# Kernel tuning notes

Hardware: AMD Instinct MI355X
Metric: run time of the kernel (lower is better)

The kernel has to match this reference:

```python
import jax, jax.numpy as jnp
import numpy as np

B, T, C, H = 1, 4096, 768, 12
D = C // H  # 64


def setup_inputs() -> dict:
    key = jax.random.key(0)
    k1, k2, k3, k4, k5 = jax.random.split(key, 5)
    x = jax.random.normal(k1, (B, T, C), dtype=jnp.float32)
    # causal mask: 1.0 where attention is DISALLOWED (strict upper triangle)
    mask = (1.0 - jnp.tril(jnp.ones((T, T), dtype=jnp.float32)))[None, None, :, :]
    s_attn = 1.0 / np.sqrt(C)
    W_qkv = jax.random.normal(k2, (C, 3 * C), dtype=jnp.float32) * s_attn
    b_qkv = jnp.zeros((3 * C,), dtype=jnp.float32)
    W_proj = jax.random.normal(k3, (C, C), dtype=jnp.float32) * s_attn
    b_proj = jnp.zeros((C,), dtype=jnp.float32)
    return {"x": x, "mask": mask, "W_qkv": W_qkv, "b_qkv": b_qkv,
            "W_proj": W_proj, "b_proj": b_proj}


def reference(x, mask, W_qkv, b_qkv, W_proj, b_proj):
    qkv = jnp.einsum('btc,cf->btf', x, W_qkv) + b_qkv        # [B,T,3C]
    q, k, v = jnp.split(qkv, 3, axis=2)
    # [B,T,C] -> [B,H,T,D]
    q = q.reshape(B, T, H, D).transpose(0, 2, 1, 3)
    k = k.reshape(B, T, H, D).transpose(0, 2, 1, 3)
    v = v.reshape(B, T, H, D).transpose(0, 2, 1, 3)
    att = jnp.einsum('bhqd,bhkd->bhqk', q, k) * (1.0 / jnp.sqrt(jnp.float32(D)))
    att = att + mask * (-1e9)
    att = jax.nn.softmax(att, axis=-1)                        # [B,H,T,T]
    y = jnp.einsum('bhqk,bhkd->bhqd', att, v)                 # [B,H,T,D]
    y = y.transpose(0, 2, 1, 3).reshape(B, T, C)
    return jnp.einsum('btc,cf->btf', y, W_proj) + b_proj
```

## Files before the change

kernel.cpp:

```cpp
#include <hip/hip_runtime.h>
#include <hip/hip_bf16.h>

typedef unsigned short u16t;
typedef short bf16x8 __attribute__((ext_vector_type(8)));
typedef short bf16x4 __attribute__((ext_vector_type(4)));
typedef float f32x4 __attribute__((ext_vector_type(4)));

#define T_SEQ 4096
#define NH    12
#define HD    64
#define C3    2304
#define CDIM  768
#define STRIP_KV 512
#define SLOTS 144
#define SC_F  0.18033688011112042f

__device__ __forceinline__ float bf2f(u16t u) {
  union { unsigned int i; float f; } c; c.i = ((unsigned int)u) << 16; return c.f;
}
__device__ __forceinline__ u16t f2bf(float f) {
  union { float f; unsigned int i; } c; c.f = f;
  unsigned int u = c.i;
  u += 0x7fffu + ((u >> 16) & 1u);
  return (u16t)(u >> 16);
}
__device__ __forceinline__ unsigned pk2bf(float a, float b) {
  __hip_bfloat162 h = __float22bfloat162_rn(make_float2(a, b));
  union { __hip_bfloat162 h; unsigned u; } c; c.h = h; return c.u;
}
__device__ __forceinline__ void gload16(const u16t* g, u16t* l) {
  __builtin_amdgcn_global_load_lds((const __attribute__((address_space(1))) void*)g,
                                   (__attribute__((address_space(3))) void*)l,
                                   16, 0, 0);
}

#define BARRIER_LGKM() __asm__ __volatile__("s_waitcnt lgkmcnt(0)\n\ts_barrier" ::: "memory")

__global__ __launch_bounds__(256) void prep_inputs(const float* __restrict__ x,
                                                   const float* __restrict__ Wqkv,
                                                   const float* __restrict__ Wproj,
                                                   u16t* __restrict__ xbf,
                                                   u16t* __restrict__ WqkvT,
                                                   u16t* __restrict__ WprojT) {
  const int z = blockIdx.z;
  const int tx = threadIdx.x, ty = threadIdx.y;
  if (z == 2) {
    const int t = ty * 32 + tx;
    const int n8 = T_SEQ * CDIM / 8;
    const int i = ((int)blockIdx.y * (int)gridDim.x + (int)blockIdx.x) * 256 + t;
    if (i < n8) {
      const float4 a = ((const float4*)x)[2 * i];
      const float4 b = ((const float4*)x)[2 * i + 1];
      union { uint4 u; unsigned w[4]; } o;
      o.w[0] = pk2bf(a.x, a.y); o.w[1] = pk2bf(a.z, a.w);
      o.w[2] = pk2bf(b.x, b.y); o.w[3] = pk2bf(b.z, b.w);
      ((uint4*)xbf)[i] = o.u;
    }
    return;
  }
  __shared__ u16t tile[32][33];
  const int Cc = z ? CDIM : C3;
  if (z && blockIdx.x >= (unsigned)(CDIM / 32)) return;
  const float* in = z ? Wproj : Wqkv;
  u16t* out = z ? WprojT : WqkvT;
  const int c0 = blockIdx.x * 32, r0 = blockIdx.y * 32;
#pragma unroll
  for (int i = 0; i < 32; i += 8)
    tile[ty + i][tx] = f2bf(in[(size_t)(r0 + ty + i) * Cc + c0 + tx]);
  __syncthreads();
#pragma unroll
  for (int i = 0; i < 32; i += 8)
    out[(size_t)(c0 + ty + i) * CDIM + r0 + tx] = tile[tx][ty + i];
}

template <int MT, int NF, bool OUTF32>
__global__ __launch_bounds__(256) void gemm_bt_bias(
    const u16t* __restrict__ A, const u16t* __restrict__ Bt,
    const float* __restrict__ bias, void* __restrict__ Cout,
    int M, int N, int K, int qcols, float qscale) {
  constexpr int BN = 32 * NF;
  constexpr int MI = MT / 32;
  constexpr int LA = MT / 64;
  constexpr int LB = NF / 2;
  constexpr int L  = LA + LB;
  __shared__ u16t lA[3][MT * 32];
  __shared__ u16t lB[3][BN * 32];
  const int t = threadIdx.x;
  const int lane = t & 63;
  const int wid  = t >> 6;
  const int quad = lane >> 4, l16 = lane & 15;

  const int gx = gridDim.x;
  const int nwg = gx * (int)gridDim.y;
  int bid = (int)blockIdx.y * gx + (int)blockIdx.x;
  if ((nwg & 7) == 0) bid = (bid & 7) * (nwg >> 3) + (bid >> 3);
  const int m0 = (bid / gx) * MT, n0 = (bid % gx) * BN;

  const int wm = (wid >> 1) * (16 * MI), wn = (wid & 1) * (16 * NF);
  const int rswz = (quad ^ ((l16 >> 1) & 3)) * 8;

  f32x4 acc[MI][NF];
#pragma unroll
  for (int i = 0; i < MI; ++i)
#pragma unroll
    for (int j = 0; j < NF; ++j) acc[i][j] = (f32x4){0.f, 0.f, 0.f, 0.f};

  auto stage = [&](int b, int k0) {
#pragma unroll
    for (int rd = 0; rd < LA; ++rd) {
      const int e = rd * 256 + t;
      const int row = e >> 2;
      const int ch  = (e & 3) ^ ((row >> 1) & 3);
      gload16(A + (size_t)(m0 + row) * K + k0 + ch * 8, &lA[b][e * 8]);
    }
#pragma unroll
    for (int rd = 0; rd < LB; ++rd) {
      const int e = rd * 256 + t;
      const int row = e >> 2;
      const int ch  = (e & 3) ^ ((row >> 1) & 3);
      gload16(Bt + (size_t)(n0 + row) * K + k0 + ch * 8, &lB[b][e * 8]);
    }
  };
  auto compute = [&](int b) {
    bf16x8 af[MI], bfr[NF];
#pragma unroll
    for (int i = 0; i < MI; ++i)
      af[i] = *(const bf16x8*)&lA[b][(wm + i * 16 + l16) * 32 + rswz];
#pragma unroll
    for (int i = 0; i < NF; ++i)
      bfr[i] = *(const bf16x8*)&lB[b][(wn + i * 16 + l16) * 32 + rswz];
#pragma unroll
    for (int i = 0; i < MI; ++i)
#pragma unroll
      for (int j = 0; j < NF; ++j)
        acc[i][j] = __builtin_amdgcn_mfma_f32_16x16x32_bf16(af[i], bfr[j], acc[i][j], 0, 0, 0);
  };

  const int NT = K >> 5;
  stage(0, 0);
  stage(1, 32);
  for (int tt = 0; tt < NT; ++tt) {
    if (tt < NT - 1) {
      __asm__ __volatile__("s_waitcnt vmcnt(%0)" :: "n"(L) : "memory");
    } else {
      __asm__ __volatile__("s_waitcnt vmcnt(0)" ::: "memory");
    }
    __builtin_amdgcn_s_barrier();
    __builtin_amdgcn_sched_barrier(0);
    compute(tt % 3);
    if (tt + 2 < NT) stage((tt + 2) % 3, (tt + 2) * 32);
  }

#pragma unroll
  for (int j = 0; j < NF; ++j) {
    const int col = n0 + wn + j * 16 + l16;
    const float bv = bias[col];
    const float cs = (col < qcols) ? qscale : 1.0f;
#pragma unroll
    for (int i = 0; i < MI; ++i) {
      const int rowb = m0 + wm + i * 16 + quad * 4;
#pragma unroll
      for (int r = 0; r < 4; ++r) {
        const float val = (acc[i][j][r] + bv) * cs;
        const size_t idx = (size_t)(rowb + r) * N + col;
        if (OUTF32) ((float*)Cout)[idx] = val;
        else        ((u16t*)Cout)[idx] = f2bf(val);
      }
    }
  }
}

#define KSTR 88
#define VSTR 88

__global__ __launch_bounds__(256, 4) void attn_partial(const u16t* __restrict__ qkv,
                                                       u16t* __restrict__ pO,
                                                       float* __restrict__ pL) {
  const int h     = blockIdx.x;
  const int strip = blockIdx.y;
  const int qt    = 31 - (int)blockIdx.z;
  const int q0 = qt * 128;
  const int kv_begin = strip * STRIP_KV;
  const int kv_end   = q0 + 128;
  if (kv_begin >= kv_end) return;
  const int kv_stop = (kv_begin + STRIP_KV < kv_end) ? kv_begin + STRIP_KV : kv_end;
  const int a = qt >> 2, b = qt & 3;
  const int slot = (a + 1) * (2 * a + b) + strip;

  __shared__ u16t lK[64 * KSTR];
  __shared__ u16t lVt[64 * VSTR];

  const int t = threadIdx.x;
  const int lane = t & 63;
  const int wid  = t >> 6;
  const int quad = lane >> 4, l16 = lane & 15;
  const int wr = q0 + wid * 32;

  const int krow = t >> 3, kcol = (t & 7) * 8;
  const int vk0 = 4 * (t >> 4);
  const int vd0 = 4 * (t & 15);
  const int vswz = (t & 3) << 3;
  const u16t* Kbase = qkv + CDIM + h * HD;
  const u16t* Vbase = qkv + 2 * CDIM + h * HD;

  bf16x8 qf[2][2];
#pragma unroll
  for (int qn = 0; qn < 2; ++qn) {
    const int row = wr + qn * 16 + l16;
#pragma unroll
    for (int kd = 0; kd < 2; ++kd)
      qf[qn][kd] = *(const bf16x8*)(qkv + (size_t)row * C3 + h * HD + kd * 32 + quad * 8);
  }

  f32x4 oaccT[4][2];
  f32x4 laccT[2];
#pragma unroll
  for (int dn = 0; dn < 4; ++dn)
#pragma unroll
    for (int qn = 0; qn < 2; ++qn) oaccT[dn][qn] = (f32x4){0.f, 0.f, 0.f, 0.f};
#pragma unroll
  for (int qn = 0; qn < 2; ++qn) laccT[qn] = (f32x4){0.f, 0.f, 0.f, 0.f};
  bf16x4 ones4;
#pragma unroll
  for (int i = 0; i < 4; ++i) ones4[i] = (short)0x3F80;

  const int pswz = ((l16 >> 2) & 3) << 3;

  uint4 kreg0, kreg1;
  union { uint2 u; u16t hw[4]; } vreg[4];

#define LOAD_TILE(KV0)                                                        \
  do {                                                                        \
    kreg0 = *(const uint4*)(Kbase + (size_t)((KV0) + krow) * C3 + kcol);      \
    kreg1 = *(const uint4*)(Kbase + (size_t)((KV0) + krow + 32) * C3 + kcol); \
    _Pragma("unroll")                                                         \
    for (int i = 0; i < 4; ++i)                                               \
      vreg[i].u = *(const uint2*)(Vbase + (size_t)((KV0) + vk0 + i) * C3 + vd0); \
  } while (0)

#define STORE_TILE()                                                          \
  do {                                                                        \
    *(uint4*)&lK[krow * KSTR + kcol] = kreg0;                                 \
    *(uint4*)&lK[(krow + 32) * KSTR + kcol] = kreg1;                          \
    _Pragma("unroll")                                                         \
    for (int j = 0; j < 4; ++j) {                                             \
      union { uint2 u; u16t hw[4]; } w;                                       \
      w.hw[0] = vreg[0].hw[j]; w.hw[1] = vreg[1].hw[j];                       \
      w.hw[2] = vreg[2].hw[j]; w.hw[3] = vreg[3].hw[j];                       \
      *(uint2*)&lVt[(vd0 + j) * VSTR + (vk0 ^ vswz)] = w.u;                   \
    }                                                                         \
  } while (0)

  LOAD_TILE(kv_begin);
  STORE_TILE();

  for (int kv0 = kv_begin; kv0 < kv_stop; kv0 += 64) {
    const bool havenext = (kv0 + 64 < kv_stop);
    if (havenext) LOAD_TILE(kv0 + 64);
    BARRIER_LGKM();

    if (kv0 <= wr + 31) {
      __builtin_amdgcn_s_setprio(1);
      f32x4 sacc[4][2];
#pragma unroll
      for (int kvt = 0; kvt < 4; ++kvt) {
        bf16x8 kf0 = *(const bf16x8*)&lK[(kvt * 16 + l16) * KSTR + quad * 8];
        bf16x8 kf1 = *(const bf16x8*)&lK[(kvt * 16 + l16) * KSTR + 32 + quad * 8];
#pragma unroll
        for (int qn = 0; qn < 2; ++qn) {
          f32x4 s = (f32x4){0.f, 0.f, 0.f, 0.f};
          s = __builtin_amdgcn_mfma_f32_16x16x32_bf16(kf0, qf[qn][0], s, 0, 0, 0);
          s = __builtin_amdgcn_mfma_f32_16x16x32_bf16(kf1, qf[qn][1], s, 0, 0, 0);
          sacc[kvt][qn] = s;
        }
      }
      const bool need_mask = (kv0 + 63 > wr);
      bf16x4 pbf[4][2];
#pragma unroll
      for (int kvt = 0; kvt < 4; ++kvt)
#pragma unroll
        for (int qn = 0; qn < 2; ++qn) {
          const int qg = wr + qn * 16 + l16;
          float pv[4];
#pragma unroll
          for (int r = 0; r < 4; ++r) {
            const int kvg = kv0 + kvt * 16 + quad * 4 + r;
            float p = __builtin_amdgcn_exp2f(sacc[kvt][qn][r]);
            if (need_mask && (kvg > qg)) p = 0.f;
            pv[r] = p;
          }
          union { bf16x4 v; unsigned u[2]; } pw;
          pw.u[0] = pk2bf(pv[0], pv[1]);
          pw.u[1] = pk2bf(pv[2], pv[3]);
          pbf[kvt][qn] = pw.v;
        }
#pragma unroll
      for (int kvt = 0; kvt < 4; ++kvt) {
        const int kvcol = (kvt * 16 + quad * 4) ^ pswz;
#pragma unroll
        for (int qn = 0; qn < 2; ++qn)
          laccT[qn] = __builtin_amdgcn_mfma_f32_16x16x16bf16_1k(
              ones4, pbf[kvt][qn], laccT[qn], 0, 0, 0);
#pragma unroll
        for (int dn = 0; dn < 4; ++dn) {
          bf16x4 vf = *(const bf16x4*)&lVt[(dn * 16 + l16) * VSTR + kvcol];
#pragma unroll
          for (int qn = 0; qn < 2; ++qn)
            oaccT[dn][qn] = __builtin_amdgcn_mfma_f32_16x16x16bf16_1k(
                vf, pbf[kvt][qn], oaccT[dn][qn], 0, 0, 0);
        }
      }
      __builtin_amdgcn_s_setprio(0);
    }
    BARRIER_LGKM();
    if (havenext) STORE_TILE();
  }

  {
    u16t* scr = &lVt[wid * 16 * 80];
    u16t* po = pO + ((size_t)h * SLOTS + slot) * 128 * HD;
    float* pl = pL + ((size_t)h * SLOTS + slot) * 128;
#pragma unroll
    for (int qn = 0; qn < 2; ++qn) {
#pragma unroll
      for (int dn = 0; dn < 4; ++dn) {
        union { bf16x4 v; unsigned u[2]; } w;
        w.u[0] = pk2bf(oaccT[dn][qn][0], oaccT[dn][qn][1]);
        w.u[1] = pk2bf(oaccT[dn][qn][2], oaccT[dn][qn][3]);
        *(bf16x4*)&scr[l16 * 80 + dn * 16 + quad * 4] = w.v;
      }
      __asm__ __volatile__("s_waitcnt lgkmcnt(0)" ::: "memory");
      const int ql = wid * 32 + qn * 16 + l16;
      uint4 w0 = *(const uint4*)&scr[l16 * 80 + quad * 16];
      uint4 w1 = *(const uint4*)&scr[l16 * 80 + quad * 16 + 8];
      u16t* dst = po + (size_t)ql * HD + quad * 16;
      *(uint4*)dst = w0;
      *(uint4*)(dst + 8) = w1;
      if (quad == 0) pl[ql] = laccT[qn][0];
      __asm__ __volatile__("s_waitcnt lgkmcnt(0)" ::: "memory");
    }
  }
#undef LOAD_TILE
#undef STORE_TILE
}

__global__ __launch_bounds__(256) void attn_normalize(const u16t* __restrict__ pO,
                                                      const float* __restrict__ pL,
                                                      u16t* __restrict__ y) {
  const int i = blockIdx.x * 256 + threadIdx.x;
  const int q = i / (CDIM / 8), c8 = (i % (CDIM / 8)) * 8;
  const int h = c8 >> 6, d = c8 & 63;
  const int qt = q >> 7, ql = q & 127;
  const int a = qt >> 2, b = qt & 3;
  const int base = (a + 1) * (2 * a + b);
  const int ns = a + 1;
  float o[8] = {0.f, 0.f, 0.f, 0.f, 0.f, 0.f, 0.f, 0.f};
  float l = 0.f;
  for (int s = 0; s < ns; ++s) {
    const size_t sl = (size_t)h * SLOTS + base + s;
    union { uint4 u; u16t hw[8]; } v;
    v.u = *(const uint4*)&pO[(sl * 128 + ql) * HD + d];
#pragma unroll
    for (int j = 0; j < 8; ++j) o[j] += bf2f(v.hw[j]);
    l += pL[sl * 128 + ql];
  }
  const float rl = 1.0f / l;
  union { uint4 u; unsigned w[4]; } wv;
#pragma unroll
  for (int j = 0; j < 4; ++j)
    wv.w[j] = pk2bf(o[2 * j] * rl, o[2 * j + 1] * rl);
  *(uint4*)&y[(size_t)q * CDIM + c8] = wv.u;
}

extern "C" void kernel_launch(void* const* d_in, const int* in_sizes, int n_in,
                              void* d_out, int out_size, void* d_ws, size_t ws_size,
                              hipStream_t stream) {
  const float* x     = (const float*)d_in[0];
  const float* Wqkv  = (const float*)d_in[2];
  const float* bqkv  = (const float*)d_in[3];
  const float* Wproj = (const float*)d_in[4];
  const float* bproj = (const float*)d_in[5];

  u16t* qkv    = (u16t*)d_ws;
  u16t* ybuf   = qkv    + (size_t)T_SEQ * C3;
  u16t* WqkvT  = ybuf   + (size_t)T_SEQ * CDIM;
  u16t* WprojT = WqkvT  + (size_t)C3 * CDIM;
  u16t* pO     = WprojT + (size_t)CDIM * CDIM;
  float* pL    = (float*)(pO + (size_t)NH * SLOTS * 128 * HD);

  prep_inputs<<<dim3(C3 / 32, CDIM / 32, 3), dim3(32, 8), 0, stream>>>(
      x, Wqkv, Wproj, ybuf, WqkvT, WprojT);
  gemm_bt_bias<128, 4, false><<<dim3(C3 / 128, T_SEQ / 128), 256, 0, stream>>>(
      ybuf, WqkvT, bqkv, qkv, T_SEQ, C3, CDIM, CDIM, SC_F);
  attn_partial<<<dim3(NH, 8, T_SEQ / 128), 256, 0, stream>>>(qkv, pO, pL);
  attn_normalize<<<(T_SEQ * CDIM / 8) / 256, 256, 0, stream>>>(pO, pL, ybuf);
  gemm_bt_bias<128, 2, true><<<dim3(CDIM / 64, T_SEQ / 128), 256, 0, stream>>>(
      ybuf, WprojT, bproj, d_out, T_SEQ, CDIM, CDIM, 0, 1.0f);
}
```

Baseline: 214.5 us.

## Split attention block across 8 waves with 16 query rows each

The attention partial kernel now runs 512 threads (8 waves) per block. Each wave owns 16 query rows instead of 32, and K/V tile loading is spread over twice as many threads. The goal is more latency hiding and smaller per-wave register state, so more waves can overlap MFMA with softmax and LDS traffic. The cost is that each K/V fragment read from LDS feeds half as many MFMAs, and barriers now synchronise more waves. The epilogue scratch also spills into the K buffer for waves 4-7.

```diff
diff --git a/kernel.cpp b/kernel.cpp
--- a/kernel.cpp
+++ b/kernel.cpp
@@ -173,7 +173,7 @@
 #define KSTR 88
 #define VSTR 88
 
-__global__ __launch_bounds__(256, 4) void attn_partial(const u16t* __restrict__ qkv,
+__global__ __launch_bounds__(512, 4) void attn_partial(const u16t* __restrict__ qkv,
                                                        u16t* __restrict__ pO,
                                                        float* __restrict__ pL) {
   const int h     = blockIdx.x;
@@ -194,60 +194,50 @@
   const int lane = t & 63;
   const int wid  = t >> 6;
   const int quad = lane >> 4, l16 = lane & 15;
-  const int wr = q0 + wid * 32;
+  const int wr = q0 + wid * 16;
 
   const int krow = t >> 3, kcol = (t & 7) * 8;
-  const int vk0 = 4 * (t >> 4);
+  const int vk0 = 2 * (t >> 4);
   const int vd0 = 4 * (t & 15);
   const int vswz = (t & 3) << 3;
   const u16t* Kbase = qkv + CDIM + h * HD;
   const u16t* Vbase = qkv + 2 * CDIM + h * HD;
 
-  bf16x8 qf[2][2];
-#pragma unroll
-  for (int qn = 0; qn < 2; ++qn) {
-    const int row = wr + qn * 16 + l16;
-#pragma unroll
-    for (int kd = 0; kd < 2; ++kd)
-      qf[qn][kd] = *(const bf16x8*)(qkv + (size_t)row * C3 + h * HD + kd * 32 + quad * 8);
-  }
-
-  f32x4 oaccT[4][2];
-  f32x4 laccT[2];
-#pragma unroll
-  for (int dn = 0; dn < 4; ++dn)
-#pragma unroll
-    for (int qn = 0; qn < 2; ++qn) oaccT[dn][qn] = (f32x4){0.f, 0.f, 0.f, 0.f};
-#pragma unroll
-  for (int qn = 0; qn < 2; ++qn) laccT[qn] = (f32x4){0.f, 0.f, 0.f, 0.f};
+  bf16x8 qf[2];
+#pragma unroll
+  for (int kd = 0; kd < 2; ++kd)
+    qf[kd] = *(const bf16x8*)(qkv + (size_t)(wr + l16) * C3 + h * HD + kd * 32 + quad * 8);
+
+  f32x4 oaccT[4];
+  f32x4 laccT;
+#pragma unroll
+  for (int dn = 0; dn < 4; ++dn) oaccT[dn] = (f32x4){0.f, 0.f, 0.f, 0.f};
+  laccT = (f32x4){0.f, 0.f, 0.f, 0.f};
   bf16x4 ones4;
 #pragma unroll
   for (int i = 0; i < 4; ++i) ones4[i] = (short)0x3F80;
 
   const int pswz = ((l16 >> 2) & 3) << 3;
 
-  uint4 kreg0, kreg1;
-  union { uint2 u; u16t hw[4]; } vreg[4];
+  uint4 kreg0;
+  union { uint2 u; u16t hw[4]; } vreg[2];
 
 #define LOAD_TILE(KV0)                                                        \
   do {                                                                        \
     kreg0 = *(const uint4*)(Kbase + (size_t)((KV0) + krow) * C3 + kcol);      \
-    kreg1 = *(const uint4*)(Kbase + (size_t)((KV0) + krow + 32) * C3 + kcol); \
     _Pragma("unroll")                                                         \
-    for (int i = 0; i < 4; ++i)                                               \
+    for (int i = 0; i < 2; ++i)                                               \
       vreg[i].u = *(const uint2*)(Vbase + (size_t)((KV0) + vk0 + i) * C3 + vd0); \
   } while (0)
 
 #define STORE_TILE()                                                          \
   do {                                                                        \
     *(uint4*)&lK[krow * KSTR + kcol] = kreg0;                                 \
-    *(uint4*)&lK[(krow + 32) * KSTR + kcol] = kreg1;                          \
     _Pragma("unroll")                                                         \
     for (int j = 0; j < 4; ++j) {                                             \
-      union { uint2 u; u16t hw[4]; } w;                                       \
+      union { unsigned u; u16t hw[2]; } w;                                    \
       w.hw[0] = vreg[0].hw[j]; w.hw[1] = vreg[1].hw[j];                       \
-      w.hw[2] = vreg[2].hw[j]; w.hw[3] = vreg[3].hw[j];                       \
-      *(uint2*)&lVt[(vd0 + j) * VSTR + (vk0 ^ vswz)] = w.u;                   \
+      *(unsigned*)&lVt[(vd0 + j) * VSTR + (vk0 ^ vswz)] = w.u;                \
     }                                                                         \
   } while (0)
 
@@ -259,55 +249,46 @@
     if (havenext) LOAD_TILE(kv0 + 64);
     BARRIER_LGKM();
 
-    if (kv0 <= wr + 31) {
+    if (kv0 <= wr + 15) {
       __builtin_amdgcn_s_setprio(1);
-      f32x4 sacc[4][2];
+      f32x4 sacc[4];
 #pragma unroll
       for (int kvt = 0; kvt < 4; ++kvt) {
         bf16x8 kf0 = *(const bf16x8*)&lK[(kvt * 16 + l16) * KSTR + quad * 8];
         bf16x8 kf1 = *(const bf16x8*)&lK[(kvt * 16 + l16) * KSTR + 32 + quad * 8];
-#pragma unroll
-        for (int qn = 0; qn < 2; ++qn) {
-          f32x4 s = (f32x4){0.f, 0.f, 0.f, 0.f};
-          s = __builtin_amdgcn_mfma_f32_16x16x32_bf16(kf0, qf[qn][0], s, 0, 0, 0);
-          s = __builtin_amdgcn_mfma_f32_16x16x32_bf16(kf1, qf[qn][1], s, 0, 0, 0);
-          sacc[kvt][qn] = s;
-        }
+        f32x4 s = (f32x4){0.f, 0.f, 0.f, 0.f};
+        s = __builtin_amdgcn_mfma_f32_16x16x32_bf16(kf0, qf[0], s, 0, 0, 0);
+        s = __builtin_amdgcn_mfma_f32_16x16x32_bf16(kf1, qf[1], s, 0, 0, 0);
+        sacc[kvt] = s;
       }
       const bool need_mask = (kv0 + 63 > wr);
-      bf16x4 pbf[4][2];
-#pragma unroll
-      for (int kvt = 0; kvt < 4; ++kvt)
-#pragma unroll
-        for (int qn = 0; qn < 2; ++qn) {
-          const int qg = wr + qn * 16 + l16;
-          float pv[4];
-#pragma unroll
-          for (int r = 0; r < 4; ++r) {
-            const int kvg = kv0 + kvt * 16 + quad * 4 + r;
-            float p = __builtin_amdgcn_exp2f(sacc[kvt][qn][r]);
-            if (need_mask && (kvg > qg)) p = 0.f;
-            pv[r] = p;
-          }
-          union { bf16x4 v; unsigned u[2]; } pw;
-          pw.u[0] = pk2bf(pv[0], pv[1]);
-          pw.u[1] = pk2bf(pv[2], pv[3]);
-          pbf[kvt][qn] = pw.v;
+      bf16x4 pbf[4];
+#pragma unroll
+      for (int kvt = 0; kvt < 4; ++kvt) {
+        const int qg = wr + l16;
+        float pv[4];
+#pragma unroll
+        for (int r = 0; r < 4; ++r) {
+          const int kvg = kv0 + kvt * 16 + quad * 4 + r;
+          float p = __builtin_amdgcn_exp2f(sacc[kvt][r]);
+          if (need_mask && (kvg > qg)) p = 0.f;
+          pv[r] = p;
         }
+        union { bf16x4 v; unsigned u[2]; } pw;
+        pw.u[0] = pk2bf(pv[0], pv[1]);
+        pw.u[1] = pk2bf(pv[2], pv[3]);
+        pbf[kvt] = pw.v;
+      }
 #pragma unroll
       for (int kvt = 0; kvt < 4; ++kvt) {
         const int kvcol = (kvt * 16 + quad * 4) ^ pswz;
-#pragma unroll
-        for (int qn = 0; qn < 2; ++qn)
-          laccT[qn] = __builtin_amdgcn_mfma_f32_16x16x16bf16_1k(
-              ones4, pbf[kvt][qn], laccT[qn], 0, 0, 0);
+        laccT = __builtin_amdgcn_mfma_f32_16x16x16bf16_1k(
+            ones4, pbf[kvt], laccT, 0, 0, 0);
 #pragma unroll
         for (int dn = 0; dn < 4; ++dn) {
           bf16x4 vf = *(const bf16x4*)&lVt[(dn * 16 + l16) * VSTR + kvcol];
-#pragma unroll
-          for (int qn = 0; qn < 2; ++qn)
-            oaccT[dn][qn] = __builtin_amdgcn_mfma_f32_16x16x16bf16_1k(
-                vf, pbf[kvt][qn], oaccT[dn][qn], 0, 0, 0);
+          oaccT[dn] = __builtin_amdgcn_mfma_f32_16x16x16bf16_1k(
+              vf, pbf[kvt], oaccT[dn], 0, 0, 0);
         }
       }
       __builtin_amdgcn_s_setprio(0);
@@ -317,28 +298,24 @@
   }
 
   {
-    u16t* scr = &lVt[wid * 16 * 80];
+    u16t* scr = (wid < 4) ? &lVt[wid * 16 * 80] : &lK[(wid - 4) * 16 * 80];
     u16t* po = pO + ((size_t)h * SLOTS + slot) * 128 * HD;
     float* pl = pL + ((size_t)h * SLOTS + slot) * 128;
 #pragma unroll
-    for (int qn = 0; qn < 2; ++qn) {
-#pragma unroll
-      for (int dn = 0; dn < 4; ++dn) {
-        union { bf16x4 v; unsigned u[2]; } w;
-        w.u[0] = pk2bf(oaccT[dn][qn][0], oaccT[dn][qn][1]);
-        w.u[1] = pk2bf(oaccT[dn][qn][2], oaccT[dn][qn][3]);
-        *(bf16x4*)&scr[l16 * 80 + dn * 16 + quad * 4] = w.v;
-      }
-      __asm__ __volatile__("s_waitcnt lgkmcnt(0)" ::: "memory");
-      const int ql = wid * 32 + qn * 16 + l16;
-      uint4 w0 = *(const uint4*)&scr[l16 * 80 + quad * 16];
-      uint4 w1 = *(const uint4*)&scr[l16 * 80 + quad * 16 + 8];
-      u16t* dst = po + (size_t)ql * HD + quad * 16;
-      *(uint4*)dst = w0;
-      *(uint4*)(dst + 8) = w1;
-      if (quad == 0) pl[ql] = laccT[qn][0];
-      __asm__ __volatile__("s_waitcnt lgkmcnt(0)" ::: "memory");
-    }
+    for (int dn = 0; dn < 4; ++dn) {
+      union { bf16x4 v; unsigned u[2]; } w;
+      w.u[0] = pk2bf(oaccT[dn][0], oaccT[dn][1]);
+      w.u[1] = pk2bf(oaccT[dn][2], oaccT[dn][3]);
+      *(bf16x4*)&scr[l16 * 80 + dn * 16 + quad * 4] = w.v;
+    }
+    __asm__ __volatile__("s_waitcnt lgkmcnt(0)" ::: "memory");
+    const int ql = wid * 16 + l16;
+    uint4 w0 = *(const uint4*)&scr[l16 * 80 + quad * 16];
+    uint4 w1 = *(const uint4*)&scr[l16 * 80 + quad * 16 + 8];
+    u16t* dst = po + (size_t)ql * HD + quad * 16;
+    *(uint4*)dst = w0;
+    *(uint4*)(dst + 8) = w1;
+    if (quad == 0) pl[ql] = laccT[0];
   }
 #undef LOAD_TILE
 #undef STORE_TILE
@@ -392,7 +369,7 @@
       x, Wqkv, Wproj, ybuf, WqkvT, WprojT);
   gemm_bt_bias<128, 4, false><<<dim3(C3 / 128, T_SEQ / 128), 256, 0, stream>>>(
       ybuf, WqkvT, bqkv, qkv, T_SEQ, C3, CDIM, CDIM, SC_F);
-  attn_partial<<<dim3(NH, 8, T_SEQ / 128), 256, 0, stream>>>(qkv, pO, pL);
+  attn_partial<<<dim3(NH, 8, T_SEQ / 128), 512, 0, stream>>>(qkv, pO, pL);
   attn_normalize<<<(T_SEQ * CDIM / 8) / 256, 256, 0, stream>>>(pO, pL, ybuf);
   gemm_bt_bias<128, 2, true><<<dim3(CDIM / 64, T_SEQ / 128), 256, 0, stream>>>(
       ybuf, WprojT, bproj, d_out, T_SEQ, CDIM, CDIM, 0, 1.0f);
```

New measurement: 219.8 us. 1.02x slower.
